# Kernel optimization log

Hardware: AMD Instinct MI355X
Metric: run time of the kernel (lower is better)

## Reference

```python
import jax, jax.numpy as jnp
import numpy as np


def _compute_deltas(ts, m):
    """Affine time-decay recurrence: delta_0 = 0; for t>=1:
    delta_t = gap_t + (1 - m_{t-1}) * delta_{t-1}, with gap broadcast over features.
    ts: [b, s] timestamps, m: [b, s, f] float 0/1 mask. Returns [b, s, f]."""
    b, s, f = m.shape
    gaps = ts[:, 1:] - ts[:, :-1]          # [b, s-1]
    a = 1.0 - m[:, :-1, :]                 # [b, s-1, f] decay coefficient

    def step(d, inp):
        g_t, a_t = inp                      # g_t: [b], a_t: [b, f]
        d = g_t[:, None] + a_t * d
        return d, d

    gT = jnp.swapaxes(gaps, 0, 1)          # [s-1, b]
    aT = jnp.swapaxes(a, 0, 1)             # [s-1, b, f]
    _, ds = jax.lax.scan(step, jnp.zeros((b, f), ts.dtype), (gT, aT))
    ds = jnp.swapaxes(ds, 0, 1)            # [b, s-1, f]
    return jnp.concatenate([jnp.zeros((b, 1, f), ts.dtype), ds], axis=1)


def setup_inputs() -> dict:
    key = jax.random.key(0)
    k1, k2, k3 = jax.random.split(key, 3)
    b, s, f = 32, 2048, 768
    # monotonically increasing timestamps (cumsum of positive gaps)
    gaps = jax.random.uniform(k1, (b, s), minval=1.0, maxval=60.0, dtype=jnp.float32)
    timestamps = jnp.cumsum(gaps, axis=1)
    encoded_data = jax.random.normal(k2, (b, s, f), dtype=jnp.float32)
    masks = jax.random.randint(k3, (b, s, f), 0, 2, dtype=jnp.int32)
    return {"timestamps": timestamps, "encoded_data": encoded_data, "masks": masks}


def reference(timestamps, encoded_data, masks):
    """JAX translation of _prepare_brits_data. Returns stacked
    [forward_deltas, backward_deltas, backward_X] of shape [3, b, s, f].
    (forward X / masks are pass-through inputs; backward mask is flip(masks).)"""
    m = masks.astype(timestamps.dtype)
    forward_deltas = _compute_deltas(timestamps, m)
    ts_b = jnp.flip(timestamps, axis=1)
    m_b = jnp.flip(m, axis=1)
    backward_deltas = jnp.abs(_compute_deltas(ts_b, m_b))
    x_b = jnp.flip(encoded_data, axis=1)
    return jnp.stack([forward_deltas, backward_deltas, x_b], axis=0)
```

## Files before the change

### kernel.cpp

```cpp
#include <hip/hip_runtime.h>
#include <stdint.h>

static constexpr int B = 32, S = 2048, F = 768;
static constexpr int CS = 64;
static constexpr int NCH = S / CS;
static constexpr int F4 = F / 4;
static constexpr int FT = F4;
static constexpr int NPAIR = B * NCH;

typedef float v4f __attribute__((ext_vector_type(4)));
typedef int   v4i __attribute__((ext_vector_type(4)));
typedef unsigned int v4u __attribute__((ext_vector_type(4)));

__device__ __forceinline__ v4f mk4(float a, float b, float c, float d) {
    v4f v; v.x = a; v.y = b; v.z = c; v.w = d; return v;
}

__global__ __launch_bounds__(FT) void passA(const v4i* __restrict__ masks,
                                            uint32_t* __restrict__ bwLo,
                                            uint32_t* __restrict__ bwHi) {
    const int hb = blockIdx.x;
    const int pair = hb >> 1, half = hb & 1;
    const int b = pair >> 5, c = pair & 31;
    const int j = threadIdx.x;
    const int r0 = c * CS + half * 32;
    const v4i* mp = masks + (size_t)(b * S + r0) * F4 + j;
    uint32_t w0 = 0, w1 = 0, w2 = 0, w3 = 0;
    #pragma unroll
    for (int g = 0; g < 4; ++g) {
        v4i mv[8];
        #pragma unroll
        for (int q = 0; q < 8; ++q) mv[q] = __builtin_nontemporal_load(&mp[(size_t)(g * 8 + q) * F4]);
        #pragma unroll
        for (int q = 0; q < 8; ++q) {
            const uint32_t bit = 1u << (g * 8 + q);
            if (mv[q].x) w0 |= bit;
            if (mv[q].y) w1 |= bit;
            if (mv[q].z) w2 |= bit;
            if (mv[q].w) w3 |= bit;
        }
    }
    v4u w; w.x = w0; w.y = w1; w.z = w2; w.w = w3;
    uint32_t* base = half ? bwHi : bwLo;
    *reinterpret_cast<v4u*>(base + (size_t)pair * F + 4 * j) = w;
}

__global__ __launch_bounds__(FT) void passC(const float* __restrict__ ts,
                                            const uint32_t* __restrict__ bwLo,
                                            const uint32_t* __restrict__ bwHi,
                                            float* __restrict__ out) {
    const int blk = blockIdx.x;
    const bool bwd = blk >= NPAIR;
    const int pair = bwd ? blk - NPAIR : blk;
    const int b = pair >> 5, c = pair & 31;
    const int g0 = c * CS;
    const int j = threadIdx.x;
    const size_t N4 = (size_t)B * S * F4;
    const float* tsb = ts + (size_t)b * S;

    __shared__ float tss[CS];
    if (j < CS) tss[j] = tsb[g0 + j];
    __syncthreads();

    v4u lo4 = *reinterpret_cast<const v4u*>(bwLo + (size_t)pair * F + 4 * j);
    v4u hi4 = *reinterpret_cast<const v4u*>(bwHi + (size_t)pair * F + 4 * j);
    uint32_t alo[4] = {lo4.x, lo4.y, lo4.z, lo4.w};
    uint32_t ahi[4] = {hi4.x, hi4.y, hi4.z, hi4.w};

    if (!bwd) {
        float p[4];
        float def = tsb[0];
        p[0] = p[1] = p[2] = p[3] = def;
        uint32_t need = 0xFu;
        for (int d = c - 1; d >= 0 && need; --d) {
            v4u ul = *reinterpret_cast<const v4u*>(bwLo + (size_t)(b * NCH + d) * F + 4 * j);
            v4u uh = *reinterpret_cast<const v4u*>(bwHi + (size_t)(b * NCH + d) * F + 4 * j);
            uint32_t lo[4] = {ul.x, ul.y, ul.z, ul.w};
            uint32_t hi[4] = {uh.x, uh.y, uh.z, uh.w};
            const int base = d * CS;
            #pragma unroll
            for (int i = 0; i < 4; ++i) if (need & (1u << i)) {
                if (hi[i])      { p[i] = tsb[base + 32 + (31 - __clz((int)hi[i]))]; need &= ~(1u << i); }
                else if (lo[i]) { p[i] = tsb[base +      (31 - __clz((int)lo[i]))]; need &= ~(1u << i); }
            }
        }
        v4f* o0 = reinterpret_cast<v4f*>(out) + (size_t)(b * S + g0) * F4 + j;
        #pragma unroll
        for (int k = 0; k < 32; ++k) {
            float t = tss[k];
            __builtin_nontemporal_store(mk4(t - p[0], t - p[1], t - p[2], t - p[3]), &o0[(size_t)k * F4]);
            const uint32_t bit = 1u << k;
            #pragma unroll
            for (int i = 0; i < 4; ++i) if (alo[i] & bit) p[i] = t;
        }
        #pragma unroll
        for (int k = 32; k < 64; ++k) {
            float t = tss[k];
            __builtin_nontemporal_store(mk4(t - p[0], t - p[1], t - p[2], t - p[3]), &o0[(size_t)k * F4]);
            const uint32_t bit = 1u << (k - 32);
            #pragma unroll
            for (int i = 0; i < 4; ++i) if (ahi[i] & bit) p[i] = t;
        }
    } else {
        float n[4];
        float def = tsb[S - 1];
        n[0] = n[1] = n[2] = n[3] = def;
        uint32_t need = 0xFu;
        for (int d = c + 1; d < NCH && need; ++d) {
            v4u ul = *reinterpret_cast<const v4u*>(bwLo + (size_t)(b * NCH + d) * F + 4 * j);
            v4u uh = *reinterpret_cast<const v4u*>(bwHi + (size_t)(b * NCH + d) * F + 4 * j);
            uint32_t lo[4] = {ul.x, ul.y, ul.z, ul.w};
            uint32_t hi[4] = {uh.x, uh.y, uh.z, uh.w};
            const int base = d * CS;
            #pragma unroll
            for (int i = 0; i < 4; ++i) if (need & (1u << i)) {
                if (lo[i])      { n[i] = tsb[base +      (__ffs((int)lo[i]) - 1)]; need &= ~(1u << i); }
                else if (hi[i]) { n[i] = tsb[base + 32 + (__ffs((int)hi[i]) - 1)]; need &= ~(1u << i); }
            }
        }
        v4f* o1b = reinterpret_cast<v4f*>(out) + N4 + (size_t)b * S * F4 + j;
        #pragma unroll
        for (int k = 63; k >= 32; --k) {
            float t = tss[k];
            size_t fr = (size_t)(S - 1 - g0 - k) * F4;
            __builtin_nontemporal_store(mk4(n[0] - t, n[1] - t, n[2] - t, n[3] - t), &o1b[fr]);
            const uint32_t bit = 1u << (k - 32);
            #pragma unroll
            for (int i = 0; i < 4; ++i) if (ahi[i] & bit) n[i] = t;
        }
        #pragma unroll
        for (int k = 31; k >= 0; --k) {
            float t = tss[k];
            size_t fr = (size_t)(S - 1 - g0 - k) * F4;
            __builtin_nontemporal_store(mk4(n[0] - t, n[1] - t, n[2] - t, n[3] - t), &o1b[fr]);
            const uint32_t bit = 1u << k;
            #pragma unroll
            for (int i = 0; i < 4; ++i) if (alo[i] & bit) n[i] = t;
        }
    }
}

static constexpr int CPY_BLOCKS = 2048;
__global__ __launch_bounds__(256) void copyK(const v4f* __restrict__ x,
                                             v4f* __restrict__ o2) {
    const size_t N4 = (size_t)B * S * F4;
    const size_t stride = (size_t)CPY_BLOCKS * 256;
    for (size_t i = (size_t)blockIdx.x * 256 + threadIdx.x; i < N4; i += stride) {
        size_t row = i / F4;
        size_t f   = i - row * F4;
        size_t t   = row & (S - 1);
        size_t src = (row - t + (S - 1 - t)) * F4 + f;
        __builtin_nontemporal_store(__builtin_nontemporal_load(&x[src]), &o2[i]);
    }
}

__global__ __launch_bounds__(FT) void deltaProbeK(const float* __restrict__ ts,
                                                  const int4* __restrict__ masks,
                                                  float* __restrict__ out) {
    const int pair = blockIdx.x;
    const int b = pair >> 5, sc = pair & 31;
    const int g0 = sc * CS;
    const int j = threadIdx.x;
    const size_t N4 = (size_t)B * S * F4;
    const float* tsb = ts + (size_t)b * S;
    const int4* mbase = masks + (size_t)b * S * F4 + j;
    __shared__ float tss[CS];
    if (j < CS) tss[j] = tsb[g0 + j];
    __syncthreads();
    uint32_t a0 = 0, a1 = 0, a2 = 0, a3 = 0, c0 = 0, c1 = 0, c2 = 0, c3 = 0;
    #pragma unroll
    for (int g = 0; g < 8; ++g) {
        int4 mv[8];
        #pragma unroll
        for (int q = 0; q < 8; ++q) mv[q] = mbase[(size_t)(g0 + g * 8 + q) * F4];
        #pragma unroll
        for (int q = 0; q < 8; ++q) {
            const int k = g * 8 + q;
            const uint32_t bit = 1u << (k & 31);
            if (k < 32) { if (mv[q].x) a0 |= bit; if (mv[q].y) a1 |= bit; if (mv[q].z) a2 |= bit; if (mv[q].w) a3 |= bit; }
            else        { if (mv[q].x) c0 |= bit; if (mv[q].y) c1 |= bit; if (mv[q].z) c2 |= bit; if (mv[q].w) c3 |= bit; }
        }
    }
    float t0v = tsb[0];
    float p0 = t0v, p1 = t0v, p2 = t0v, p3 = t0v;
    if (g0 > 0) {
        unsigned um = 0xFu; int r = g0 - 1;
        while (um && r >= 0) {
            int rl = (r - 7 > 0) ? r - 7 : 0; int nn = r - rl + 1;
            int4 mv[8];
            #pragma unroll
            for (int q = 0; q < 8; ++q) if (q < nn) mv[q] = mbase[(size_t)(r - q) * F4];
            #pragma unroll
            for (int q = 0; q < 8; ++q) if (q < nn) {
                float t = tsb[r - q];
                if ((um & 1u) && mv[q].x) { p0 = t; um &= ~1u; }
                if ((um & 2u) && mv[q].y) { p1 = t; um &= ~2u; }
                if ((um & 4u) && mv[q].z) { p2 = t; um &= ~4u; }
                if ((um & 8u) && mv[q].w) { p3 = t; um &= ~8u; }
            }
            r = rl - 1;
        }
    }
    float tev = tsb[S - 1];
    float n0 = tev, n1 = tev, n2 = tev, n3 = tev;
    if (g0 + CS < S) {
        unsigned um = 0xFu; int r = g0 + CS;
        while (um && r < S) {
            int rh = (r + 7 < S - 1) ? r + 7 : S - 1; int nn = rh - r + 1;
            int4 mv[8];
            #pragma unroll
            for (int q = 0; q < 8; ++q) if (q < nn) mv[q] = mbase[(size_t)(r + q) * F4];
            #pragma unroll
            for (int q = 0; q < 8; ++q) if (q < nn) {
                float t = tsb[r + q];
                if ((um & 1u) && mv[q].x) { n0 = t; um &= ~1u; }
                if ((um & 2u) && mv[q].y) { n1 = t; um &= ~2u; }
                if ((um & 4u) && mv[q].z) { n2 = t; um &= ~4u; }
                if ((um & 8u) && mv[q].w) { n3 = t; um &= ~8u; }
            }
            r = rh + 1;
        }
    }
    v4f* o0 = reinterpret_cast<v4f*>(out) + (size_t)(b * S + g0) * F4 + j;
    #pragma unroll
    for (int k = 0; k < 32; ++k) {
        float t = tss[k];
        __builtin_nontemporal_store(mk4(t - p0, t - p1, t - p2, t - p3), &o0[(size_t)k * F4]);
        const uint32_t bit = 1u << k;
        if (a0 & bit) p0 = t; if (a1 & bit) p1 = t; if (a2 & bit) p2 = t; if (a3 & bit) p3 = t;
    }
    #pragma unroll
    for (int k = 32; k < 64; ++k) {
        float t = tss[k];
        __builtin_nontemporal_store(mk4(t - p0, t - p1, t - p2, t - p3), &o0[(size_t)k * F4]);
        const uint32_t bit = 1u << (k - 32);
        if (c0 & bit) p0 = t; if (c1 & bit) p1 = t; if (c2 & bit) p2 = t; if (c3 & bit) p3 = t;
    }
    v4f* o1b = reinterpret_cast<v4f*>(out) + N4 + (size_t)b * S * F4 + j;
    #pragma unroll
    for (int k = 63; k >= 32; --k) {
        float t = tss[k];
        size_t fr = (size_t)(S - 1 - g0 - k) * F4;
        __builtin_nontemporal_store(mk4(n0 - t, n1 - t, n2 - t, n3 - t), &o1b[fr]);
        const uint32_t bit = 1u << (k - 32);
        if (c0 & bit) n0 = t; if (c1 & bit) n1 = t; if (c2 & bit) n2 = t; if (c3 & bit) n3 = t;
    }
    #pragma unroll
    for (int k = 31; k >= 0; --k) {
        float t = tss[k];
        size_t fr = (size_t)(S - 1 - g0 - k) * F4;
        __builtin_nontemporal_store(mk4(n0 - t, n1 - t, n2 - t, n3 - t), &o1b[fr]);
        const uint32_t bit = 1u << k;
        if (a0 & bit) n0 = t; if (a1 & bit) n1 = t; if (a2 & bit) n2 = t; if (a3 & bit) n3 = t;
    }
}

extern "C" void kernel_launch(void* const* d_in, const int* in_sizes, int n_in,
                              void* d_out, int out_size, void* d_ws, size_t ws_size,
                              hipStream_t stream) {
    const float* ts    = (const float*)d_in[0];
    const v4f* x       = (const v4f*)d_in[1];
    float* out = (float*)d_out;
    const size_t N4 = (size_t)B * S * F4;
    const size_t plane_words = (size_t)NPAIR * F;
    const size_t bw_bytes = 2 * plane_words * sizeof(uint32_t);

    if (ws_size >= bw_bytes) {
        uint32_t* bwLo = (uint32_t*)d_ws;
        uint32_t* bwHi = bwLo + plane_words;
        passA<<<2 * NPAIR, FT, 0, stream>>>((const v4i*)d_in[2], bwLo, bwHi);
        passC<<<2 * NPAIR, FT, 0, stream>>>(ts, bwLo, bwHi, out);
    } else {
        deltaProbeK<<<NPAIR, FT, 0, stream>>>(ts, (const int4*)d_in[2], out);
    }
    copyK<<<CPY_BLOCKS, 256, 0, stream>>>(x, reinterpret_cast<v4f*>(out) + 2 * N4);
}
```

Before: 194.0 us.

## Fuse mask packing, delta scan and reverse copy into one cooperative kernel

Replaces the separate mask-packing, delta-writing and reverse-copy launches with a single cooperative kernel. Each block copies its flipped slice of x, packs its mask bits into the workspace, then waits on a grid-wide barrier. After the barrier it scans neighbouring chunks' bitmasks to find the carry-in and carry-out timestamps, then writes both delta planes. The aim is to remove launch gaps and overlap the copy traffic with the mask reads. In exchange it needs all 1024 blocks resident at once for the grid sync and adds the cost of that barrier. If the cooperative launch fails it falls back to the old three-kernel path. The old fallback for a too-small workspace is removed, so in that case the delta planes are no longer written.

```diff
diff --git a/kernel.cpp b/kernel.cpp
--- a/kernel.cpp
+++ b/kernel.cpp
@@ -1,5 +1,8 @@
 #include <hip/hip_runtime.h>
+#include <hip/hip_cooperative_groups.h>
 #include <stdint.h>
+
+namespace cg = cooperative_groups;
 
 static constexpr int B = 32, S = 2048, F = 768;
 static constexpr int CS = 64;
@@ -14,6 +17,142 @@
 
 __device__ __forceinline__ v4f mk4(float a, float b, float c, float d) {
     v4f v; v.x = a; v.y = b; v.z = c; v.w = d; return v;
+}
+
+__global__ __launch_bounds__(FT, 4) void coopK(const v4i* __restrict__ masks,
+                                               const v4f* __restrict__ x,
+                                               const float* __restrict__ ts,
+                                               uint32_t* __restrict__ bwLo,
+                                               uint32_t* __restrict__ bwHi,
+                                               float* __restrict__ out) {
+    const int pair = blockIdx.x;
+    const int b = pair >> 5, c = pair & 31;
+    const int g0 = c * CS;
+    const int j = threadIdx.x;
+    const size_t N4 = (size_t)B * S * F4;
+    const float* tsb = ts + (size_t)b * S;
+
+    __shared__ float tss[CS];
+    if (j < CS) tss[j] = tsb[g0 + j];
+
+    const v4f* xb = x + (size_t)b * S * F4 + j;
+    v4f* o2 = reinterpret_cast<v4f*>(out) + 2 * N4 + (size_t)(b * S + g0) * F4 + j;
+    #pragma unroll 8
+    for (int k = 0; k < CS; ++k) {
+        __builtin_nontemporal_store(
+            __builtin_nontemporal_load(&xb[(size_t)(S - 1 - g0 - k) * F4]),
+            &o2[(size_t)k * F4]);
+    }
+
+    const v4i* mp = masks + (size_t)(b * S + g0) * F4 + j;
+    uint32_t a0 = 0, a1 = 0, a2 = 0, a3 = 0;
+    uint32_t c0 = 0, c1 = 0, c2 = 0, c3 = 0;
+    #pragma unroll
+    for (int g = 0; g < 8; ++g) {
+        v4i mv[8];
+        #pragma unroll
+        for (int q = 0; q < 8; ++q) mv[q] = __builtin_nontemporal_load(&mp[(size_t)(g * 8 + q) * F4]);
+        #pragma unroll
+        for (int q = 0; q < 8; ++q) {
+            const int k = g * 8 + q;
+            const uint32_t bit = 1u << (k & 31);
+            if (k < 32) {
+                if (mv[q].x) a0 |= bit;
+                if (mv[q].y) a1 |= bit;
+                if (mv[q].z) a2 |= bit;
+                if (mv[q].w) a3 |= bit;
+            } else {
+                if (mv[q].x) c0 |= bit;
+                if (mv[q].y) c1 |= bit;
+                if (mv[q].z) c2 |= bit;
+                if (mv[q].w) c3 |= bit;
+            }
+        }
+    }
+    {
+        v4u wl; wl.x = a0; wl.y = a1; wl.z = a2; wl.w = a3;
+        v4u wh; wh.x = c0; wh.y = c1; wh.z = c2; wh.w = c3;
+        __builtin_nontemporal_store(wl, reinterpret_cast<v4u*>(bwLo + ((size_t)pair * F + 4 * j)));
+        __builtin_nontemporal_store(wh, reinterpret_cast<v4u*>(bwHi + ((size_t)pair * F + 4 * j)));
+    }
+
+    cg::this_grid().sync();
+
+    uint32_t alo[4] = {a0, a1, a2, a3};
+    uint32_t ahi[4] = {c0, c1, c2, c3};
+    float p[4], n[4];
+    {
+        float def = tsb[0];
+        p[0] = p[1] = p[2] = p[3] = def;
+        uint32_t need = 0xFu;
+        for (int d = c - 1; d >= 0 && need; --d) {
+            v4u ul = *reinterpret_cast<const v4u*>(bwLo + ((size_t)(b * NCH + d) * F + 4 * j));
+            v4u uh = *reinterpret_cast<const v4u*>(bwHi + ((size_t)(b * NCH + d) * F + 4 * j));
+            uint32_t lo[4] = {ul.x, ul.y, ul.z, ul.w};
+            uint32_t hi[4] = {uh.x, uh.y, uh.z, uh.w};
+            const int base = d * CS;
+            #pragma unroll
+            for (int i = 0; i < 4; ++i) if (need & (1u << i)) {
+                if (hi[i])      { p[i] = tsb[base + 32 + (31 - __clz((int)hi[i]))]; need &= ~(1u << i); }
+                else if (lo[i]) { p[i] = tsb[base +      (31 - __clz((int)lo[i]))]; need &= ~(1u << i); }
+            }
+        }
+    }
+    {
+        float def = tsb[S - 1];
+        n[0] = n[1] = n[2] = n[3] = def;
+        uint32_t need = 0xFu;
+        for (int d = c + 1; d < NCH && need; ++d) {
+            v4u ul = *reinterpret_cast<const v4u*>(bwLo + ((size_t)(b * NCH + d) * F + 4 * j));
+            v4u uh = *reinterpret_cast<const v4u*>(bwHi + ((size_t)(b * NCH + d) * F + 4 * j));
+            uint32_t lo[4] = {ul.x, ul.y, ul.z, ul.w};
+            uint32_t hi[4] = {uh.x, uh.y, uh.z, uh.w};
+            const int base = d * CS;
+            #pragma unroll
+            for (int i = 0; i < 4; ++i) if (need & (1u << i)) {
+                if (lo[i])      { n[i] = tsb[base +      (__ffs((int)lo[i]) - 1)]; need &= ~(1u << i); }
+                else if (hi[i]) { n[i] = tsb[base + 32 + (__ffs((int)hi[i]) - 1)]; need &= ~(1u << i); }
+            }
+        }
+    }
+
+    v4f* o0 = reinterpret_cast<v4f*>(out) + (size_t)(b * S + g0) * F4 + j;
+    #pragma unroll
+    for (int k = 0; k < 32; ++k) {
+        float t = tss[k];
+        __builtin_nontemporal_store(mk4(t - p[0], t - p[1], t - p[2], t - p[3]), &o0[(size_t)k * F4]);
+        const uint32_t bit = 1u << k;
+        #pragma unroll
+        for (int i = 0; i < 4; ++i) if (alo[i] & bit) p[i] = t;
+    }
+    #pragma unroll
+    for (int k = 32; k < 64; ++k) {
+        float t = tss[k];
+        __builtin_nontemporal_store(mk4(t - p[0], t - p[1], t - p[2], t - p[3]), &o0[(size_t)k * F4]);
+        const uint32_t bit = 1u << (k - 32);
+        #pragma unroll
+        for (int i = 0; i < 4; ++i) if (ahi[i] & bit) p[i] = t;
+    }
+
+    v4f* o1b = reinterpret_cast<v4f*>(out) + N4 + (size_t)b * S * F4 + j;
+    #pragma unroll
+    for (int k = 63; k >= 32; --k) {
+        float t = tss[k];
+        size_t fr = (size_t)(S - 1 - g0 - k) * F4;
+        __builtin_nontemporal_store(mk4(n[0] - t, n[1] - t, n[2] - t, n[3] - t), &o1b[fr]);
+        const uint32_t bit = 1u << (k - 32);
+        #pragma unroll
+        for (int i = 0; i < 4; ++i) if (ahi[i] & bit) n[i] = t;
+    }
+    #pragma unroll
+    for (int k = 31; k >= 0; --k) {
+        float t = tss[k];
+        size_t fr = (size_t)(S - 1 - g0 - k) * F4;
+        __builtin_nontemporal_store(mk4(n[0] - t, n[1] - t, n[2] - t, n[3] - t), &o1b[fr]);
+        const uint32_t bit = 1u << k;
+        #pragma unroll
+        for (int i = 0; i < 4; ++i) if (alo[i] & bit) n[i] = t;
+    }
 }
 
 __global__ __launch_bounds__(FT) void passA(const v4i* __restrict__ masks,
@@ -154,112 +293,12 @@
     }
 }
 
-__global__ __launch_bounds__(FT) void deltaProbeK(const float* __restrict__ ts,
-                                                  const int4* __restrict__ masks,
-                                                  float* __restrict__ out) {
-    const int pair = blockIdx.x;
-    const int b = pair >> 5, sc = pair & 31;
-    const int g0 = sc * CS;
-    const int j = threadIdx.x;
-    const size_t N4 = (size_t)B * S * F4;
-    const float* tsb = ts + (size_t)b * S;
-    const int4* mbase = masks + (size_t)b * S * F4 + j;
-    __shared__ float tss[CS];
-    if (j < CS) tss[j] = tsb[g0 + j];
-    __syncthreads();
-    uint32_t a0 = 0, a1 = 0, a2 = 0, a3 = 0, c0 = 0, c1 = 0, c2 = 0, c3 = 0;
-    #pragma unroll
-    for (int g = 0; g < 8; ++g) {
-        int4 mv[8];
-        #pragma unroll
-        for (int q = 0; q < 8; ++q) mv[q] = mbase[(size_t)(g0 + g * 8 + q) * F4];
-        #pragma unroll
-        for (int q = 0; q < 8; ++q) {
-            const int k = g * 8 + q;
-            const uint32_t bit = 1u << (k & 31);
-            if (k < 32) { if (mv[q].x) a0 |= bit; if (mv[q].y) a1 |= bit; if (mv[q].z) a2 |= bit; if (mv[q].w) a3 |= bit; }
-            else        { if (mv[q].x) c0 |= bit; if (mv[q].y) c1 |= bit; if (mv[q].z) c2 |= bit; if (mv[q].w) c3 |= bit; }
-        }
-    }
-    float t0v = tsb[0];
-    float p0 = t0v, p1 = t0v, p2 = t0v, p3 = t0v;
-    if (g0 > 0) {
-        unsigned um = 0xFu; int r = g0 - 1;
-        while (um && r >= 0) {
-            int rl = (r - 7 > 0) ? r - 7 : 0; int nn = r - rl + 1;
-            int4 mv[8];
-            #pragma unroll
-            for (int q = 0; q < 8; ++q) if (q < nn) mv[q] = mbase[(size_t)(r - q) * F4];
-            #pragma unroll
-            for (int q = 0; q < 8; ++q) if (q < nn) {
-                float t = tsb[r - q];
-                if ((um & 1u) && mv[q].x) { p0 = t; um &= ~1u; }
-                if ((um & 2u) && mv[q].y) { p1 = t; um &= ~2u; }
-                if ((um & 4u) && mv[q].z) { p2 = t; um &= ~4u; }
-                if ((um & 8u) && mv[q].w) { p3 = t; um &= ~8u; }
-            }
-            r = rl - 1;
-        }
-    }
-    float tev = tsb[S - 1];
-    float n0 = tev, n1 = tev, n2 = tev, n3 = tev;
-    if (g0 + CS < S) {
-        unsigned um = 0xFu; int r = g0 + CS;
-        while (um && r < S) {
-            int rh = (r + 7 < S - 1) ? r + 7 : S - 1; int nn = rh - r + 1;
-            int4 mv[8];
-            #pragma unroll
-            for (int q = 0; q < 8; ++q) if (q < nn) mv[q] = mbase[(size_t)(r + q) * F4];
-            #pragma unroll
-            for (int q = 0; q < 8; ++q) if (q < nn) {
-                float t = tsb[r + q];
-                if ((um & 1u) && mv[q].x) { n0 = t; um &= ~1u; }
-                if ((um & 2u) && mv[q].y) { n1 = t; um &= ~2u; }
-                if ((um & 4u) && mv[q].z) { n2 = t; um &= ~4u; }
-                if ((um & 8u) && mv[q].w) { n3 = t; um &= ~8u; }
-            }
-            r = rh + 1;
-        }
-    }
-    v4f* o0 = reinterpret_cast<v4f*>(out) + (size_t)(b * S + g0) * F4 + j;
-    #pragma unroll
-    for (int k = 0; k < 32; ++k) {
-        float t = tss[k];
-        __builtin_nontemporal_store(mk4(t - p0, t - p1, t - p2, t - p3), &o0[(size_t)k * F4]);
-        const uint32_t bit = 1u << k;
-        if (a0 & bit) p0 = t; if (a1 & bit) p1 = t; if (a2 & bit) p2 = t; if (a3 & bit) p3 = t;
-    }
-    #pragma unroll
-    for (int k = 32; k < 64; ++k) {
-        float t = tss[k];
-        __builtin_nontemporal_store(mk4(t - p0, t - p1, t - p2, t - p3), &o0[(size_t)k * F4]);
-        const uint32_t bit = 1u << (k - 32);
-        if (c0 & bit) p0 = t; if (c1 & bit) p1 = t; if (c2 & bit) p2 = t; if (c3 & bit) p3 = t;
-    }
-    v4f* o1b = reinterpret_cast<v4f*>(out) + N4 + (size_t)b * S * F4 + j;
-    #pragma unroll
-    for (int k = 63; k >= 32; --k) {
-        float t = tss[k];
-        size_t fr = (size_t)(S - 1 - g0 - k) * F4;
-        __builtin_nontemporal_store(mk4(n0 - t, n1 - t, n2 - t, n3 - t), &o1b[fr]);
-        const uint32_t bit = 1u << (k - 32);
-        if (c0 & bit) n0 = t; if (c1 & bit) n1 = t; if (c2 & bit) n2 = t; if (c3 & bit) n3 = t;
-    }
-    #pragma unroll
-    for (int k = 31; k >= 0; --k) {
-        float t = tss[k];
-        size_t fr = (size_t)(S - 1 - g0 - k) * F4;
-        __builtin_nontemporal_store(mk4(n0 - t, n1 - t, n2 - t, n3 - t), &o1b[fr]);
-        const uint32_t bit = 1u << k;
-        if (a0 & bit) n0 = t; if (a1 & bit) n1 = t; if (a2 & bit) n2 = t; if (a3 & bit) n3 = t;
-    }
-}
-
 extern "C" void kernel_launch(void* const* d_in, const int* in_sizes, int n_in,
                               void* d_out, int out_size, void* d_ws, size_t ws_size,
                               hipStream_t stream) {
     const float* ts    = (const float*)d_in[0];
     const v4f* x       = (const v4f*)d_in[1];
+    const v4i* masks   = (const v4i*)d_in[2];
     float* out = (float*)d_out;
     const size_t N4 = (size_t)B * S * F4;
     const size_t plane_words = (size_t)NPAIR * F;
@@ -268,10 +307,15 @@
     if (ws_size >= bw_bytes) {
         uint32_t* bwLo = (uint32_t*)d_ws;
         uint32_t* bwHi = bwLo + plane_words;
-        passA<<<2 * NPAIR, FT, 0, stream>>>((const v4i*)d_in[2], bwLo, bwHi);
+        void* args[] = {(void*)&masks, (void*)&x, (void*)&ts,
+                        (void*)&bwLo, (void*)&bwHi, (void*)&out};
+        hipError_t e = hipLaunchCooperativeKernel((const void*)coopK, dim3(NPAIR), dim3(FT),
+                                                  args, 0, stream);
+        if (e == hipSuccess) return;
+        passA<<<2 * NPAIR, FT, 0, stream>>>(masks, bwLo, bwHi);
         passC<<<2 * NPAIR, FT, 0, stream>>>(ts, bwLo, bwHi, out);
-    } else {
-        deltaProbeK<<<NPAIR, FT, 0, stream>>>(ts, (const int4*)d_in[2], out);
+        copyK<<<CPY_BLOCKS, 256, 0, stream>>>(x, reinterpret_cast<v4f*>(out) + 2 * N4);
+        return;
     }
     copyK<<<CPY_BLOCKS, 256, 0, stream>>>(x, reinterpret_cast<v4f*>(out) + 2 * N4);
 }
```

After: 370.0 us. +90.7%, slower.
